# Kernel optimization log

Hardware: AMD Instinct MI355X
Metric: run time of the kernel (lower is better)

The kernel has to match this reference:

```python
import jax, jax.numpy as jnp
import numpy as np

B, S, D, K = 32, 512, 768, 3


def setup_inputs() -> dict:
    key = jax.random.key(0)
    ks = jax.random.split(key, 6)
    hidden = jax.random.normal(ks[0], (B, S, D), jnp.float32)
    weights_sub = jax.random.normal(ks[1], (B, S, D), jnp.float32)
    obj_target = jax.random.randint(ks[2], (B, S), 0, K, jnp.int32)
    W_cnn = jax.random.normal(ks[3], (2 * D, D), jnp.float32) * 0.02  # Conv1D k=1 == dense
    b_cnn = jnp.zeros((D,), jnp.float32)
    W_dense = jax.random.normal(ks[4], (D, K), jnp.float32) * 0.02
    b_dense = jnp.zeros((K,), jnp.float32)
    trans = jax.random.uniform(ks[5], (K, K), jnp.float32)  # tf.random.uniform init
    return dict(hidden=hidden, weights_sub=weights_sub, W_cnn=W_cnn, b_cnn=b_cnn,
                W_dense=W_dense, b_dense=b_dense, trans=trans, obj_target=obj_target)


def _crf(logits, trans, obj_target, seq_len):
    Bn, Sn, Kn = logits.shape
    pos = jnp.arange(Sn)

    first = logits[:, 0]                              # [B,K]
    rest = jnp.transpose(logits[:, 1:], (1, 0, 2))    # [S-1,B,K]

    # ---- log-norm via forward algorithm (tfa-style: unmasked scan, gather last valid alpha)
    def fwd_step(alpha, inp):
        new = inp + jax.nn.logsumexp(alpha[:, :, None] + trans[None], axis=1)
        return new, new

    _, alphas = jax.lax.scan(fwd_step, first, rest)               # [S-1,B,K]
    all_alphas = jnp.concatenate([first[None], alphas], axis=0)   # [S,B,K]
    idx = jnp.clip(seq_len - 1, 0, Sn - 1)
    alpha_last = all_alphas[idx, jnp.arange(Bn)]                  # [B,K]
    log_norm = jax.nn.logsumexp(alpha_last, axis=-1)
    log_norm = jnp.where(seq_len <= 0, 0.0, log_norm)

    # ---- gold-path score
    mask_u = pos[None, :] < seq_len[:, None]
    unary = jnp.sum(jnp.take_along_axis(logits, obj_target[..., None], axis=-1)[..., 0]
                    * mask_u, axis=1)
    mask_b = pos[None, :-1] < (seq_len - 1)[:, None]
    binary = jnp.sum(trans[obj_target[:, :-1], obj_target[:, 1:]] * mask_b, axis=1)
    log_likelihood = unary + binary - log_norm

    # ---- Viterbi decode (masked forward + backtrace)
    mask = pos[None, :] < seq_len[:, None]

    def vit_step(alpha, xs):
        pot_t, m_t = xs
        scores = alpha[:, :, None] + trans[None]      # [B, K_prev, K_cur]
        bp = jnp.argmax(scores, axis=1).astype(jnp.int32)
        new = pot_t + jnp.max(scores, axis=1)
        alpha = jnp.where(m_t[:, None], new, alpha)
        bp = jnp.where(m_t[:, None], bp, 0)
        return alpha, bp

    final_alpha, bps = jax.lax.scan(vit_step, first,
                                    (rest, jnp.transpose(mask[:, 1:])))  # bps: [S-1,B,K]
    # bp_full[t][b, k] = best previous tag at t-1 given tag k at t
    bp_full = jnp.concatenate([jnp.zeros((1, Bn, Kn), jnp.int32), bps], axis=0)
    init_tag = jnp.argmax(final_alpha, axis=-1).astype(jnp.int32)
    Lm1 = seq_len - 1

    def back_step(prev_tag, t):
        bp_next = bp_full[jnp.minimum(t + 1, Sn - 1)]                    # [B,K]
        from_bp = jnp.take_along_axis(bp_next, prev_tag[:, None], axis=1)[:, 0]
        tag = jnp.where(t == Lm1, init_tag, jnp.where(t < Lm1, from_bp, 0))
        return tag, tag

    _, tags_rev = jax.lax.scan(back_step, jnp.zeros((Bn,), jnp.int32),
                               jnp.arange(Sn - 1, -1, -1))
    tags = jnp.transpose(tags_rev[::-1])  # [B,S]
    return tags, log_likelihood


def reference(hidden, weights_sub, W_cnn, b_cnn, W_dense, b_dense, trans, obj_target):
    seq_len = jnp.sum((obj_target >= 1).astype(jnp.int32), axis=1)  # as in source
    x = jnp.concatenate([hidden, weights_sub], axis=-1)             # [B,S,2D]
    h = jnp.einsum('bsd,df->bsf', x, W_cnn) + b_cnn                 # Conv1D kernel_size=1
    logits = jnp.einsum('bsf,fk->bsk', h, W_dense) + b_dense        # [B,S,K]
    return _crf(logits, trans, obj_target, seq_len)
```

## Files before the change

kernel.cpp:

```cpp
#include <hip/hip_runtime.h>
#include <cstdint>
#include <cstddef>


#define DF 768
#define DX 1536
#define NINF 1e30f

__device__ __forceinline__ float lse3(float x, float y, float z) {
  float m = fmaxf(x, fmaxf(y, z));
  return m + __logf(__expf(x - m) + __expf(y - m) + __expf(z - m));
}

__device__ __forceinline__ void lse_compose(const float* A, const float* B, float* R) {
#pragma unroll
  for (int i = 0; i < 3; ++i)
#pragma unroll
    for (int j = 0; j < 3; ++j)
      R[3 * i + j] = lse3(A[3 * i + 0] + B[0 + j], A[3 * i + 1] + B[3 + j], A[3 * i + 2] + B[6 + j]);
}

__device__ __forceinline__ void max_compose(const float* A, const float* B, float* R) {
#pragma unroll
  for (int i = 0; i < 3; ++i)
#pragma unroll
    for (int j = 0; j < 3; ++j)
      R[3 * i + j] = fmaxf(fmaxf(A[3 * i + 0] + B[0 + j], A[3 * i + 1] + B[3 + j]), A[3 * i + 2] + B[6 + j]);
}

__device__ __forceinline__ int map_compose(int a, int b) {
  int r = 0;
#pragma unroll
  for (int j = 0; j < 3; ++j) r |= ((a >> (2 * ((b >> (2 * j)) & 3))) & 3) << (2 * j);
  return r;
}

__device__ __forceinline__ unsigned long long shfl_down_u64(unsigned long long v, int d) {
  int lo = __shfl_down((int)(unsigned int)(v & 0xffffffffULL), d, 64);
  int hi = __shfl_down((int)(unsigned int)(v >> 32), d, 64);
  return ((unsigned long long)(unsigned int)hi << 32) | (unsigned long long)(unsigned int)lo;
}

__global__ __launch_bounds__(64) void k_weff(
    const float* __restrict__ Wc, const float* __restrict__ bc,
    const float* __restrict__ Wd, const float* __restrict__ bd,
    float* __restrict__ WeffT, float* __restrict__ beff) {
  int r = blockIdx.x;
  int lane = threadIdx.x;
  const float* src = (r < DX) ? (Wc + (size_t)r * DF) : bc;
  float a0 = 0.f, a1 = 0.f, a2 = 0.f;
  for (int f = lane; f < DF; f += 64) {
    float w = src[f];
    const float* wd = Wd + f * 3;
    a0 += w * wd[0]; a1 += w * wd[1]; a2 += w * wd[2];
  }
#pragma unroll
  for (int off = 32; off; off >>= 1) {
    a0 += __shfl_xor(a0, off, 64);
    a1 += __shfl_xor(a1, off, 64);
    a2 += __shfl_xor(a2, off, 64);
  }
  if (lane == 0) {
    if (r < DX) {
      WeffT[0 * DX + r] = a0; WeffT[1 * DX + r] = a1; WeffT[2 * DX + r] = a2;
    } else {
      beff[0] = a0 + bd[0]; beff[1] = a1 + bd[1]; beff[2] = a2 + bd[2];
    }
  }
}

__global__ __launch_bounds__(256) void k_logits(
    const float* __restrict__ hidden, const float* __restrict__ wsub,
    const float* __restrict__ WeffT, const float* __restrict__ beff,
    float* __restrict__ logits) {
  __shared__ float smem[8 * 1536];
  const int lane = threadIdx.x & 63;
  const int wv = threadIdx.x >> 6;

  float4 wr[3][6];
  {
    const float4* wt4 = (const float4*)WeffT;
#pragma unroll
    for (int k = 0; k < 3; ++k)
#pragma unroll
      for (int c = 0; c < 6; ++c)
        wr[k][c] = wt4[k * 384 + 64 * c + lane];
  }
  float b0 = beff[0], b1 = beff[1], b2 = beff[2];

  for (int tile = blockIdx.x; tile < 2048; tile += gridDim.x) {
    const int row0 = tile * 8;
#pragma unroll
    for (int i = 0; i < 12; ++i) {
      int c = wv * 12 + i;
      int row = c / 6, cr = c % 6;
      int half = cr / 3, part = cr % 3;
      const float* g = (half ? wsub : hidden) + (size_t)(row0 + row) * DF + part * 256 + lane * 4;
      float* l = smem + row * 1536 + half * 768 + part * 256;
      __builtin_amdgcn_global_load_lds((const __attribute__((address_space(1))) void*)g,
                                       (__attribute__((address_space(3))) void*)l, 16, 0, 0);
    }
    __builtin_amdgcn_s_waitcnt(0);
    __syncthreads();

#pragma unroll
    for (int rr = 0; rr < 2; ++rr) {
      int r = wv * 2 + rr;
      const float4* slot = (const float4*)(smem + r * 1536);
      float a0 = 0.f, a1 = 0.f, a2 = 0.f;
#pragma unroll
      for (int c = 0; c < 6; ++c) {
        float4 v = slot[64 * c + lane];
        a0 += v.x * wr[0][c].x + v.y * wr[0][c].y + v.z * wr[0][c].z + v.w * wr[0][c].w;
        a1 += v.x * wr[1][c].x + v.y * wr[1][c].y + v.z * wr[1][c].z + v.w * wr[1][c].w;
        a2 += v.x * wr[2][c].x + v.y * wr[2][c].y + v.z * wr[2][c].z + v.w * wr[2][c].w;
      }
#pragma unroll
      for (int s = 32; s; s >>= 1) {
        a0 += __shfl_xor(a0, s, 64);
        a1 += __shfl_xor(a1, s, 64);
        a2 += __shfl_xor(a2, s, 64);
      }
      if (lane == 0) {
        float* o = logits + (size_t)(row0 + r) * 3;
        o[0] = a0 + b0; o[1] = a1 + b1; o[2] = a2 + b2;
      }
    }
    __syncthreads();
  }
}

__global__ __launch_bounds__(128) void k_crf(
    const float* __restrict__ logits, const float* __restrict__ trans,
    const int* __restrict__ tgt, float* __restrict__ out) {
  const int b = blockIdx.x;
  const int lane = threadIdx.x & 63;
  const int wv = threadIdx.x >> 6;
  const float* lrow = logits + (size_t)b * 1536;

  float lg[24];
  {
    const float4* l4 = (const float4*)(lrow + lane * 24);
#pragma unroll
    for (int i = 0; i < 6; ++i) {
      float4 v = l4[i];
      lg[4 * i + 0] = v.x; lg[4 * i + 1] = v.y; lg[4 * i + 2] = v.z; lg[4 * i + 3] = v.w;
    }
  }
  int tl[8];
  {
    const int4* t4 = (const int4*)(tgt + (size_t)b * 512 + lane * 8);
    int4 u = t4[0], v = t4[1];
    tl[0] = u.x; tl[1] = u.y; tl[2] = u.z; tl[3] = u.w;
    tl[4] = v.x; tl[5] = v.y; tl[6] = v.z; tl[7] = v.w;
  }
  int cnt = 0;
#pragma unroll
  for (int j = 0; j < 8; ++j) cnt += (tl[j] >= 1) ? 1 : 0;
#pragma unroll
  for (int s = 32; s; s >>= 1) cnt += __shfl_xor(cnt, s, 64);
  const int L = cnt;

  float T[9];
#pragma unroll
  for (int i = 0; i < 9; ++i) T[i] = trans[i];
  float f0 = lrow[0], f1 = lrow[1], f2 = lrow[2];

  if (wv == 0) {
    float part = 0.f;
    int tln = __shfl_down(tl[0], 1, 64);
#pragma unroll
    for (int j = 0; j < 8; ++j) {
      int t = 8 * lane + j;
      if (t < L) part += lg[3 * j + tl[j]];
      int nxt = (j < 7) ? tl[j + 1] : tln;
      if (t < L - 1) part += T[3 * tl[j] + nxt];
    }
#pragma unroll
    for (int s = 32; s; s >>= 1) part += __shfl_xor(part, s, 64);

    int idx = L - 1; if (idx < 0) idx = 0;
    float C[9] = {0.f, -NINF, -NINF, -NINF, 0.f, -NINF, -NINF, -NINF, 0.f};
#pragma unroll
    for (int j = 0; j < 8; ++j) {
      int t = 8 * lane + j;
      if (t >= 1 && t <= idx) {
        float M[9], R[9];
#pragma unroll
        for (int i = 0; i < 3; ++i)
#pragma unroll
          for (int k = 0; k < 3; ++k) M[3 * i + k] = T[3 * i + k] + lg[3 * j + k];
        lse_compose(C, M, R);
#pragma unroll
        for (int i = 0; i < 9; ++i) C[i] = R[i];
      }
    }
#pragma unroll
    for (int s = 1; s < 64; s <<= 1) {
      float D[9], A[9], Bm[9], R[9];
#pragma unroll
      for (int i = 0; i < 9; ++i) D[i] = __shfl_xor(C[i], s, 64);
      bool hi = (lane & s) != 0;
#pragma unroll
      for (int i = 0; i < 9; ++i) { A[i] = hi ? D[i] : C[i]; Bm[i] = hi ? C[i] : D[i]; }
      lse_compose(A, Bm, R);
#pragma unroll
      for (int i = 0; i < 9; ++i) C[i] = R[i];
    }
    float al0 = lse3(f0 + C[0], f1 + C[3], f2 + C[6]);
    float al1 = lse3(f0 + C[1], f1 + C[4], f2 + C[7]);
    float al2 = lse3(f0 + C[2], f1 + C[5], f2 + C[8]);
    float log_norm = lse3(al0, al1, al2);
    if (L <= 0) log_norm = 0.f;
    if (lane == 0) out[16384 + b] = part - log_norm;
  } else {
    float P[9] = {0.f, -NINF, -NINF, -NINF, 0.f, -NINF, -NINF, -NINF, 0.f};
#pragma unroll
    for (int j = 0; j < 8; ++j) {
      int t = 8 * lane + j;
      if (t >= 1 && t < L) {
        float M[9], R[9];
#pragma unroll
        for (int i = 0; i < 3; ++i)
#pragma unroll
          for (int k = 0; k < 3; ++k) M[3 * i + k] = T[3 * i + k] + lg[3 * j + k];
        max_compose(P, M, R);
#pragma unroll
        for (int i = 0; i < 9; ++i) P[i] = R[i];
      }
    }
    float S[9];
#pragma unroll
    for (int i = 0; i < 9; ++i) S[i] = P[i];
#pragma unroll
    for (int s = 1; s < 64; s <<= 1) {
      float D[9];
#pragma unroll
      for (int i = 0; i < 9; ++i) D[i] = __shfl_up(S[i], s, 64);
      if (lane >= s) {
        float R[9];
        max_compose(D, S, R);
#pragma unroll
        for (int i = 0; i < 9; ++i) S[i] = R[i];
      }
    }
    float E[9];
#pragma unroll
    for (int i = 0; i < 9; ++i) E[i] = __shfl_up(S[i], 1, 64);
    if (lane == 0) {
      E[0] = 0.f; E[1] = -NINF; E[2] = -NINF;
      E[3] = -NINF; E[4] = 0.f; E[5] = -NINF;
      E[6] = -NINF; E[7] = -NINF; E[8] = 0.f;
    }
    float a0 = fmaxf(fmaxf(f0 + E[0], f1 + E[3]), f2 + E[6]);
    float a1 = fmaxf(fmaxf(f0 + E[1], f1 + E[4]), f2 + E[7]);
    float a2 = fmaxf(fmaxf(f0 + E[2], f1 + E[5]), f2 + E[8]);

    unsigned long long vbp = 0ULL;
#pragma unroll
    for (int j = 0; j < 8; ++j) {
      int t = 8 * lane + j;
      if (t >= 1 && t < L) {
        int bpw = 0;
        float n0, n1, n2;
        {
          int bp = 0; float m = a0 + T[0]; float c1 = a1 + T[3]; if (c1 > m) { m = c1; bp = 1; }
          float c2 = a2 + T[6]; if (c2 > m) { m = c2; bp = 2; }
          n0 = lg[3 * j + 0] + m; bpw |= bp;
        }
        {
          int bp = 0; float m = a0 + T[1]; float c1 = a1 + T[4]; if (c1 > m) { m = c1; bp = 1; }
          float c2 = a2 + T[7]; if (c2 > m) { m = c2; bp = 2; }
          n1 = lg[3 * j + 1] + m; bpw |= bp << 2;
        }
        {
          int bp = 0; float m = a0 + T[2]; float c1 = a1 + T[5]; if (c1 > m) { m = c1; bp = 1; }
          float c2 = a2 + T[8]; if (c2 > m) { m = c2; bp = 2; }
          n2 = lg[3 * j + 2] + m; bpw |= bp << 4;
        }
        a0 = n0; a1 = n1; a2 = n2;
        vbp |= (unsigned long long)bpw << (6 * j);
      }
    }
    float g0 = __shfl(a0, 63, 64), g1 = __shfl(a1, 63, 64), g2 = __shfl(a2, 63, 64);
    int init_tag = 0; float mx = g0;
    if (g1 > mx) { mx = g1; init_tag = 1; }
    if (g2 > mx) { mx = g2; init_tag = 2; }

    unsigned long long nb = shfl_down_u64(vbp, 1);
    int ht[8];
#pragma unroll
    for (int j = 0; j < 8; ++j) {
      int t = 8 * lane + j;
      int h = 0x24;
      if (t < L - 1) h = (j < 7) ? (int)((vbp >> (6 * (j + 1))) & 63ULL) : (int)(nb & 63ULL);
      ht[j] = h;
    }
    int F = 0x24;
#pragma unroll
    for (int j = 7; j >= 0; --j) F = map_compose(ht[j], F);
    int S2 = F;
#pragma unroll
    for (int s = 1; s < 64; s <<= 1) {
      int D = __shfl_down(S2, s, 64);
      if (lane + s < 64) S2 = map_compose(S2, D);
    }
    int tail = __shfl_down(S2, 1, 64);
    if (lane == 63) tail = 0x24;
    int cur = (tail >> (2 * init_tag)) & 3;
    int tags[8];
#pragma unroll
    for (int j = 7; j >= 0; --j) {
      cur = (ht[j] >> (2 * cur)) & 3;
      int t = 8 * lane + j;
      tags[j] = (t < L) ? cur : 0;
    }
    float4 o0, o1;
    o0.x = (float)tags[0]; o0.y = (float)tags[1]; o0.z = (float)tags[2]; o0.w = (float)tags[3];
    o1.x = (float)tags[4]; o1.y = (float)tags[5]; o1.z = (float)tags[6]; o1.w = (float)tags[7];
    float4* op = (float4*)(out + (size_t)b * 512 + lane * 8);
    op[0] = o0; op[1] = o1;
  }
}

extern "C" void kernel_launch(void* const* d_in, const int* in_sizes, int n_in,
                              void* d_out, int out_size, void* d_ws, size_t ws_size,
                              hipStream_t stream) {
  const float* hidden = (const float*)d_in[0];
  const float* wsub   = (const float*)d_in[1];
  const float* Wc     = (const float*)d_in[2];
  const float* bc     = (const float*)d_in[3];
  const float* Wd     = (const float*)d_in[4];
  const float* bd     = (const float*)d_in[5];
  const float* trans  = (const float*)d_in[6];
  const int*   tgt    = (const int*)d_in[7];

  float* ws     = (float*)d_ws;
  float* WeffT  = ws;
  float* beff   = ws + 4608;
  float* logits = ws + 4624;
  float* out    = (float*)d_out;

  hipLaunchKernelGGL(k_weff,   dim3(1537), dim3(64),  0, stream, Wc, bc, Wd, bd, WeffT, beff);
  hipLaunchKernelGGL(k_logits, dim3(512),  dim3(256), 0, stream, hidden, wsub, WeffT, beff, logits);
  hipLaunchKernelGGL(k_crf,    dim3(32),   dim3(128), 0, stream, logits, trans, tgt, out);
}
```

Baseline: 149.5 us.

## Double-buffer per-wave row loads in logits kernel and pack weff rows per block

The logits kernel moves from block-wide 8-row tiles with __syncthreads to per-wave double-buffered LDS staging. Each wave issues async global-to-LDS loads for its next row while computing the current one, using partial vmcnt waits instead of full drains and barriers. The weff kernel packs four rows per 256-thread block with a fully unrolled inner loop, so far fewer blocks are launched. The risk is that the hand-encoded waitcnt values must exactly match the number of outstanding loads, or the kernel reads stale data.

```diff
diff --git a/kernel.cpp b/kernel.cpp
--- a/kernel.cpp
+++ b/kernel.cpp
@@ -41,15 +41,19 @@
   return ((unsigned long long)(unsigned int)hi << 32) | (unsigned long long)(unsigned int)lo;
 }
 
-__global__ __launch_bounds__(64) void k_weff(
+__global__ __launch_bounds__(256) void k_weff(
     const float* __restrict__ Wc, const float* __restrict__ bc,
     const float* __restrict__ Wd, const float* __restrict__ bd,
     float* __restrict__ WeffT, float* __restrict__ beff) {
-  int r = blockIdx.x;
-  int lane = threadIdx.x;
+  int lane = threadIdx.x & 63;
+  int wv = threadIdx.x >> 6;
+  int r = blockIdx.x * 4 + wv;
+  if (r > DX) return;
   const float* src = (r < DX) ? (Wc + (size_t)r * DF) : bc;
   float a0 = 0.f, a1 = 0.f, a2 = 0.f;
-  for (int f = lane; f < DF; f += 64) {
+#pragma unroll
+  for (int it = 0; it < 12; ++it) {
+    int f = lane + 64 * it;
     float w = src[f];
     const float* wd = Wd + f * 3;
     a0 += w * wd[0]; a1 += w * wd[1]; a2 += w * wd[2];
@@ -73,7 +77,7 @@
     const float* __restrict__ hidden, const float* __restrict__ wsub,
     const float* __restrict__ WeffT, const float* __restrict__ beff,
     float* __restrict__ logits) {
-  __shared__ float smem[8 * 1536];
+  __shared__ float smem[4 * 2 * 1536];
   const int lane = threadIdx.x & 63;
   const int wv = threadIdx.x >> 6;
 
@@ -86,48 +90,58 @@
       for (int c = 0; c < 6; ++c)
         wr[k][c] = wt4[k * 384 + 64 * c + lane];
   }
-  float b0 = beff[0], b1 = beff[1], b2 = beff[2];
-
-  for (int tile = blockIdx.x; tile < 2048; tile += gridDim.x) {
-    const int row0 = tile * 8;
-#pragma unroll
-    for (int i = 0; i < 12; ++i) {
-      int c = wv * 12 + i;
-      int row = c / 6, cr = c % 6;
-      int half = cr / 3, part = cr % 3;
-      const float* g = (half ? wsub : hidden) + (size_t)(row0 + row) * DF + part * 256 + lane * 4;
-      float* l = smem + row * 1536 + half * 768 + part * 256;
-      __builtin_amdgcn_global_load_lds((const __attribute__((address_space(1))) void*)g,
-                                       (__attribute__((address_space(3))) void*)l, 16, 0, 0);
-    }
-    __builtin_amdgcn_s_waitcnt(0);
-    __syncthreads();
-
-#pragma unroll
-    for (int rr = 0; rr < 2; ++rr) {
-      int r = wv * 2 + rr;
-      const float4* slot = (const float4*)(smem + r * 1536);
-      float a0 = 0.f, a1 = 0.f, a2 = 0.f;
-#pragma unroll
-      for (int c = 0; c < 6; ++c) {
-        float4 v = slot[64 * c + lane];
-        a0 += v.x * wr[0][c].x + v.y * wr[0][c].y + v.z * wr[0][c].z + v.w * wr[0][c].w;
-        a1 += v.x * wr[1][c].x + v.y * wr[1][c].y + v.z * wr[1][c].z + v.w * wr[1][c].w;
-        a2 += v.x * wr[2][c].x + v.y * wr[2][c].y + v.z * wr[2][c].z + v.w * wr[2][c].w;
-      }
-#pragma unroll
-      for (int s = 32; s; s >>= 1) {
-        a0 += __shfl_xor(a0, s, 64);
-        a1 += __shfl_xor(a1, s, 64);
-        a2 += __shfl_xor(a2, s, 64);
-      }
-      if (lane == 0) {
-        float* o = logits + (size_t)(row0 + r) * 3;
-        o[0] = a0 + b0; o[1] = a1 + b1; o[2] = a2 + b2;
-      }
-    }
-    __syncthreads();
-  }
+  const float b0 = beff[0], b1 = beff[1], b2 = beff[2];
+
+  float* mybuf = smem + wv * 3072;
+  const int slot = blockIdx.x * 4 + wv;
+
+#define STAGE(ROW, BUF)                                                              \
+  do {                                                                               \
+    const float* hsrc_ = hidden + (size_t)(ROW)*DF + lane * 4;                       \
+    const float* ssrc_ = wsub + (size_t)(ROW)*DF + lane * 4;                         \
+    float* l_ = mybuf + (BUF)*1536;                                                  \
+    _Pragma("unroll")                                                                \
+    for (int c_ = 0; c_ < 3; ++c_) {                                                 \
+      __builtin_amdgcn_global_load_lds(                                              \
+          (const __attribute__((address_space(1))) void*)(hsrc_ + c_ * 256),         \
+          (__attribute__((address_space(3))) void*)(l_ + c_ * 256), 16, 0, 0);       \
+      __builtin_amdgcn_global_load_lds(                                              \
+          (const __attribute__((address_space(1))) void*)(ssrc_ + c_ * 256),         \
+          (__attribute__((address_space(3))) void*)(l_ + 768 + c_ * 256), 16, 0, 0); \
+    }                                                                                \
+  } while (0)
+
+  STAGE(slot, 0);
+#pragma unroll
+  for (int p = 0; p < 8; ++p) {
+    if (p < 7) {
+      STAGE(slot + (p + 1) * 2048, (p + 1) & 1);
+      __builtin_amdgcn_s_waitcnt(0xF76);
+    } else {
+      __builtin_amdgcn_s_waitcnt(0xF70);
+    }
+    __builtin_amdgcn_sched_barrier(0);
+    const float4* xb = (const float4*)(mybuf + (p & 1) * 1536);
+    float a0 = 0.f, a1 = 0.f, a2 = 0.f;
+#pragma unroll
+    for (int c = 0; c < 6; ++c) {
+      float4 v = xb[64 * c + lane];
+      a0 += v.x * wr[0][c].x + v.y * wr[0][c].y + v.z * wr[0][c].z + v.w * wr[0][c].w;
+      a1 += v.x * wr[1][c].x + v.y * wr[1][c].y + v.z * wr[1][c].z + v.w * wr[1][c].w;
+      a2 += v.x * wr[2][c].x + v.y * wr[2][c].y + v.z * wr[2][c].z + v.w * wr[2][c].w;
+    }
+#pragma unroll
+    for (int s = 32; s; s >>= 1) {
+      a0 += __shfl_xor(a0, s, 64);
+      a1 += __shfl_xor(a1, s, 64);
+      a2 += __shfl_xor(a2, s, 64);
+    }
+    if (lane == 0) {
+      float* o = logits + (size_t)(slot + p * 2048) * 3;
+      o[0] = a0 + b0; o[1] = a1 + b1; o[2] = a2 + b2;
+    }
+  }
+#undef STAGE
 }
 
 __global__ __launch_bounds__(128) void k_crf(
@@ -341,7 +355,7 @@
   float* logits = ws + 4624;
   float* out    = (float*)d_out;
 
-  hipLaunchKernelGGL(k_weff,   dim3(1537), dim3(64),  0, stream, Wc, bc, Wd, bd, WeffT, beff);
-  hipLaunchKernelGGL(k_logits, dim3(512),  dim3(256), 0, stream, hidden, wsub, WeffT, beff, logits);
-  hipLaunchKernelGGL(k_crf,    dim3(32),   dim3(128), 0, stream, logits, trans, tgt, out);
-}
+  hipLaunchKernelGGL(k_weff,   dim3(385), dim3(256), 0, stream, Wc, bc, Wd, bd, WeffT, beff);
+  hipLaunchKernelGGL(k_logits, dim3(512), dim3(256), 0, stream, hidden, wsub, WeffT, beff, logits);
+  hipLaunchKernelGGL(k_crf,    dim3(32),  dim3(128), 0, stream, logits, trans, tgt, out);
+}
```

Measured after the change: 145.9 us. -2.4%, faster.
